# Kernel tuning notes

Measured on AMD Instinct MI355X. Metric: run time of the kernel, lower is better.

The kernel has to match this reference:

```python
import jax, jax.numpy as jnp
import numpy as np

HIDDEN = 64
LATENT = 32
HEADS = 4
EDGE_DIM = 3
NEG_SLOPE = 0.2
N_NODES = 50000
N_EDGES = 400000
IN_DIM = 128
NUM_CLASSES = 10
NUM_GRAPHS = 64


def _gatv2_layer(x, src, dst, edge_attr, Wl, Wr, We, att, b):
    # x: [N, F]; src/dst: [E] (self-loops already included); edge_attr: [E, 3]
    N = x.shape[0]
    xl = (x @ Wl).reshape(N, HEADS, HIDDEN)          # source transform (lin_l)
    xr = (x @ Wr).reshape(N, HEADS, HIDDEN)          # target transform (lin_r)
    e = (edge_attr @ We).reshape(-1, HEADS, HIDDEN)  # edge transform (lin_edge)
    s = jax.nn.leaky_relu(xl[src] + xr[dst] + e, NEG_SLOPE)   # [E,H,C]
    logits = jnp.einsum('ehc,hc->eh', s, att)                 # [E,H]
    # segment softmax over incoming edges of each destination node
    m = jax.ops.segment_max(logits, dst, num_segments=N)      # [N,H]
    ex = jnp.exp(logits - m[dst])
    denom = jax.ops.segment_sum(ex, dst, num_segments=N)      # [N,H]
    alpha = ex / denom[dst]                                   # [E,H]
    msg = xl[src] * alpha[:, :, None]                         # [E,H,C]
    out = jax.ops.segment_sum(msg, dst, num_segments=N)       # [N,H,C]
    return out.mean(axis=1) + b                               # concat=False -> head mean


def setup_inputs() -> dict:
    key = jax.random.key(0)
    ks = jax.random.split(key, 24)
    inp = {}
    inp['x'] = jax.random.normal(ks[0], (N_NODES, IN_DIM), dtype=jnp.float32)
    inp['edge_index'] = jax.random.randint(ks[1], (2, N_EDGES), 0, N_NODES)
    inp['edge_attr'] = jax.random.normal(ks[2], (N_EDGES, EDGE_DIM), dtype=jnp.float32)
    inp['batch'] = jnp.sort(jax.random.randint(ks[3], (N_NODES,), 0, NUM_GRAPHS))
    HC = HEADS * HIDDEN

    def glorot(k, shape):
        fan = shape[0] + shape[-1]
        return jax.random.normal(k, shape, dtype=jnp.float32) * jnp.sqrt(2.0 / fan)

    # layer 0 (in_dim -> hidden), layer 1 (hidden -> hidden)
    inp['Wl0'] = glorot(ks[4], (IN_DIM, HC)); inp['Wr0'] = glorot(ks[5], (IN_DIM, HC))
    inp['We0'] = glorot(ks[6], (EDGE_DIM, HC)); inp['att0'] = glorot(ks[7], (HEADS, HIDDEN))
    inp['b0'] = jnp.zeros((HIDDEN,), jnp.float32)
    inp['Wl1'] = glorot(ks[8], (HIDDEN, HC)); inp['Wr1'] = glorot(ks[9], (HIDDEN, HC))
    inp['We1'] = glorot(ks[10], (EDGE_DIM, HC)); inp['att1'] = glorot(ks[11], (HEADS, HIDDEN))
    inp['b1'] = jnp.zeros((HIDDEN,), jnp.float32)
    inp['W_mu'] = glorot(ks[12], (HIDDEN, LATENT)); inp['b_mu'] = jnp.zeros((LATENT,), jnp.float32)
    inp['W_dec'] = glorot(ks[13], (LATENT, IN_DIM)); inp['b_dec'] = jnp.zeros((IN_DIM,), jnp.float32)
    inp['W_cls'] = glorot(ks[14], (LATENT, NUM_CLASSES)); inp['b_cls'] = jnp.zeros((NUM_CLASSES,), jnp.float32)
    inp['weight'] = jax.random.normal(ks[15], (LATENT,), dtype=jnp.float32)
    return inp


def reference(x, edge_index, edge_attr, batch,
              Wl0, Wr0, We0, att0, b0,
              Wl1, Wr1, We1, att1, b1,
              W_mu, b_mu, W_dec, b_dec, W_cls, b_cls, weight):
    N = x.shape[0]
    # add self-loops once (PyG add_self_loops=True; edge_attr fill_value='mean')
    loops = jnp.arange(N, dtype=edge_index.dtype)
    src = jnp.concatenate([edge_index[0], loops])
    dst = jnp.concatenate([edge_index[1], loops])
    ea_mean = jnp.mean(edge_attr, axis=0)
    ea = jnp.concatenate([edge_attr, jnp.broadcast_to(ea_mean, (N, EDGE_DIM))], axis=0)

    h = jax.nn.relu(_gatv2_layer(x, src, dst, ea, Wl0, Wr0, We0, att0, b0))
    h = jax.nn.relu(_gatv2_layer(h, src, dst, ea, Wl1, Wr1, We1, att1, b1))
    z = h @ W_mu + b_mu                                   # [N, LATENT]

    recon = z @ W_dec + b_dec                             # node_recon: [N, in_dim]
    link = jnp.sum(z[edge_index[0]] * z[edge_index[1]] * weight, axis=1)  # [E]
    g_emb = jax.ops.segment_sum(z, batch, num_segments=NUM_GRAPHS)        # global_add_pool
    logits = g_emb @ W_cls + b_cls                        # [G, num_classes]
    return z, recon, link, logits
```

## Files before the change

kernel.cpp:

```cpp
#include <hip/hip_runtime.h>
#include <math.h>

#define HIDDEN 64
#define LATENT 32
#define HEADS 4
#define IN_DIM 128
#define NUM_CLASSES 10
#define NUM_GRAPHS 64
#define NEG_SLOPE 0.2f
#define HC 256

__global__ void k_easum(const float* __restrict__ ea, int E, float* __restrict__ ea_sum) {
    float s0 = 0.f, s1 = 0.f, s2 = 0.f;
    for (int e = blockIdx.x * blockDim.x + threadIdx.x; e < E; e += gridDim.x * blockDim.x) {
        s0 += ea[e * 3 + 0];
        s1 += ea[e * 3 + 1];
        s2 += ea[e * 3 + 2];
    }
    for (int off = 32; off; off >>= 1) {
        s0 += __shfl_xor(s0, off);
        s1 += __shfl_xor(s1, off);
        s2 += __shfl_xor(s2, off);
    }
    if ((threadIdx.x & 63) == 0) {
        atomicAdd(&ea_sum[0], s0);
        atomicAdd(&ea_sum[1], s1);
        atomicAdd(&ea_sum[2], s2);
    }
}

__global__ void k_hist(const int* __restrict__ ei, int* __restrict__ deg, int E0) {
    int e = blockIdx.x * blockDim.x + threadIdx.x;
    if (e < E0) atomicAdd(&deg[ei[E0 + e]], 1);
}

__global__ void k_scan1(const int* __restrict__ deg, int* __restrict__ off,
                        int* __restrict__ bsum, int N) {
    __shared__ int sh[256];
    int t = threadIdx.x, i = blockIdx.x * 256 + t;
    int v = (i < N) ? deg[i] : 0;
    sh[t] = v;
    __syncthreads();
    for (int d = 1; d < 256; d <<= 1) {
        int x = (t >= d) ? sh[t - d] : 0;
        __syncthreads();
        sh[t] += x;
        __syncthreads();
    }
    if (i < N) off[i] = sh[t] - v;
    if (t == 255) bsum[blockIdx.x] = sh[255];
}

__global__ void k_scan2(int* __restrict__ bsum, int nb) {
    __shared__ int sh[256];
    int t = threadIdx.x;
    int v = (t < nb) ? bsum[t] : 0;
    sh[t] = v;
    __syncthreads();
    for (int d = 1; d < 256; d <<= 1) {
        int x = (t >= d) ? sh[t - d] : 0;
        __syncthreads();
        sh[t] += x;
        __syncthreads();
    }
    if (t < nb) bsum[t] = sh[t] - v;
}

__global__ void k_scan3(int* __restrict__ off, const int* __restrict__ bsum,
                        int* __restrict__ cur, int N) {
    int i = blockIdx.x * 256 + threadIdx.x;
    if (i >= N) return;
    int o = off[i] + bsum[blockIdx.x];
    off[i] = o;
    cur[i] = o;
}

__global__ void k_scatter(const int* __restrict__ ei, const float* __restrict__ ea,
                          int* __restrict__ cur, int* __restrict__ csr_src,
                          float4* __restrict__ csr_a, int E0) {
    int e = blockIdx.x * blockDim.x + threadIdx.x;
    if (e >= E0) return;
    int dst = ei[E0 + e];
    int pos = atomicAdd(&cur[dst], 1);
    csr_src[pos] = ei[e];
    csr_a[pos] = make_float4(ea[e * 3], ea[e * 3 + 1], ea[e * 3 + 2], 0.f);
}

template <int K>
__global__ __launch_bounds__(256, 2) void k_gemm(const float* __restrict__ X,
                                                 const float* __restrict__ Wl,
                                                 const float* __restrict__ Wr,
                                                 float* __restrict__ xl, float* __restrict__ xr,
                                                 int N) {
    constexpr int KC = 64;
    constexpr int PAD = 132;
    __shared__ float sx[KC * PAD];

    const int M0 = blockIdx.x * 128;
    const int nt = blockIdx.y;
    const float* W = ((nt < 2) ? Wl : Wr) + (nt & 1) * 128;
    float* out = ((nt < 2) ? xl : xr) + (nt & 1) * 128;

    const int t = threadIdx.x;
    const int tr = t >> 4;
    const int tc = t & 15;

    float acc[8][8];
#pragma unroll
    for (int i = 0; i < 8; i++)
#pragma unroll
        for (int j = 0; j < 8; j++) acc[i][j] = 0.f;

    const int kq = t & 15;
    const int nsub = t >> 4;

    for (int kc0 = 0; kc0 < K; kc0 += KC) {
        __syncthreads();
#pragma unroll
        for (int pass = 0; pass < 8; ++pass) {
            int node = pass * 16 + nsub;
            int gn = M0 + node;
            float4 v = make_float4(0.f, 0.f, 0.f, 0.f);
            if (gn < N) v = ((const float4*)(X + (size_t)gn * K + kc0))[kq];
            int k = kq * 4;
            sx[(k + 0) * PAD + node] = v.x;
            sx[(k + 1) * PAD + node] = v.y;
            sx[(k + 2) * PAD + node] = v.z;
            sx[(k + 3) * PAD + node] = v.w;
        }
        __syncthreads();

        const float* Wc = W + (size_t)kc0 * HC;
#pragma unroll 4
        for (int k = 0; k < KC; ++k) {
            float4 a0 = *(const float4*)&sx[k * PAD + tr * 8];
            float4 a1 = *(const float4*)&sx[k * PAD + tr * 8 + 4];
            float4 b0 = *(const float4*)&Wc[(size_t)k * HC + tc * 8];
            float4 b1 = *(const float4*)&Wc[(size_t)k * HC + tc * 8 + 4];
            float a[8] = {a0.x, a0.y, a0.z, a0.w, a1.x, a1.y, a1.z, a1.w};
            float b[8] = {b0.x, b0.y, b0.z, b0.w, b1.x, b1.y, b1.z, b1.w};
#pragma unroll
            for (int i = 0; i < 8; i++)
#pragma unroll
                for (int j = 0; j < 8; j++) acc[i][j] += a[i] * b[j];
        }
    }

#pragma unroll
    for (int i = 0; i < 8; i++) {
        int gn = M0 + tr * 8 + i;
        if (gn < N) {
            float* p = out + (size_t)gn * HC + tc * 8;
            ((float4*)p)[0] = make_float4(acc[i][0], acc[i][1], acc[i][2], acc[i][3]);
            ((float4*)p)[1] = make_float4(acc[i][4], acc[i][5], acc[i][6], acc[i][7]);
        }
    }
}

__global__ void k_gat(const float* __restrict__ xl, const float* __restrict__ xr,
                      const int* __restrict__ csr_src, const float4* __restrict__ csr_a,
                      const int* __restrict__ off, const int* __restrict__ deg,
                      const float* __restrict__ easum, float invE,
                      const float* __restrict__ We, const float* __restrict__ att,
                      const float* __restrict__ bias, float* __restrict__ out, int N) {
    int wid = (blockIdx.x * blockDim.x + threadIdx.x) >> 6;
    int L = threadIdx.x & 63;
    if (wid >= N) return;
    int n = wid;

    float4 xr4 = ((const float4*)(xr + (size_t)n * HC))[L];
    float4 w0 = ((const float4*)We)[L];
    float4 w1 = ((const float4*)(We + HC))[L];
    float4 w2 = ((const float4*)(We + 2 * HC))[L];
    float4 at = ((const float4*)att)[L];
    float am0 = easum[0] * invE, am1 = easum[1] * invE, am2 = easum[2] * invE;

    float m = -INFINITY, d = 0.f;
    float acc0 = 0.f, acc1 = 0.f, acc2 = 0.f, acc3 = 0.f;
    int base = off[n], cnt = deg[n];

    for (int i = -1; i < cnt; i++) {
        int src;
        float a0, a1, a2;
        if (i < 0) {
            src = n;
            a0 = am0; a1 = am1; a2 = am2;
        } else {
            src = csr_src[base + i];
            float4 a = csr_a[base + i];
            a0 = a.x; a1 = a.y; a2 = a.z;
        }
        float4 xs = ((const float4*)(xl + (size_t)src * HC))[L];
        float s0 = xs.x + xr4.x + (a0 * w0.x + a1 * w1.x + a2 * w2.x);
        float s1 = xs.y + xr4.y + (a0 * w0.y + a1 * w1.y + a2 * w2.y);
        float s2 = xs.z + xr4.z + (a0 * w0.z + a1 * w1.z + a2 * w2.z);
        float s3 = xs.w + xr4.w + (a0 * w0.w + a1 * w1.w + a2 * w2.w);
        s0 = (s0 > 0.f) ? s0 : NEG_SLOPE * s0;
        s1 = (s1 > 0.f) ? s1 : NEG_SLOPE * s1;
        s2 = (s2 > 0.f) ? s2 : NEG_SLOPE * s2;
        s3 = (s3 > 0.f) ? s3 : NEG_SLOPE * s3;
        float p = s0 * at.x + s1 * at.y + s2 * at.z + s3 * at.w;
        p += __shfl_xor(p, 1);
        p += __shfl_xor(p, 2);
        p += __shfl_xor(p, 4);
        p += __shfl_xor(p, 8);
        float mn = fmaxf(m, p);
        float sc = __expf(m - mn);
        float ex = __expf(p - mn);
        d = d * sc + ex;
        acc0 = acc0 * sc + ex * xs.x;
        acc1 = acc1 * sc + ex * xs.y;
        acc2 = acc2 * sc + ex * xs.z;
        acc3 = acc3 * sc + ex * xs.w;
        m = mn;
    }
    float inv_d = 1.f / d;
    float v0 = acc0 * inv_d, v1 = acc1 * inv_d, v2 = acc2 * inv_d, v3 = acc3 * inv_d;
    v0 += __shfl_xor(v0, 16); v1 += __shfl_xor(v1, 16);
    v2 += __shfl_xor(v2, 16); v3 += __shfl_xor(v3, 16);
    v0 += __shfl_xor(v0, 32); v1 += __shfl_xor(v1, 32);
    v2 += __shfl_xor(v2, 32); v3 += __shfl_xor(v3, 32);
    if (L < 16) {
        float4 bx = ((const float4*)bias)[L];
        float4 o;
        o.x = fmaxf(0.25f * v0 + bx.x, 0.f);
        o.y = fmaxf(0.25f * v1 + bx.y, 0.f);
        o.z = fmaxf(0.25f * v2 + bx.z, 0.f);
        o.w = fmaxf(0.25f * v3 + bx.w, 0.f);
        ((float4*)(out + (size_t)n * HIDDEN))[L] = o;
    }
}

__global__ void k_mu(const float* __restrict__ h, const float* __restrict__ Wmu,
                     const float* __restrict__ bmu, float* __restrict__ z, int N) {
    int i = blockIdx.x * blockDim.x + threadIdx.x;
    if (i >= N * LATENT) return;
    int n = i >> 5, j = i & 31;
    const float* hr = h + (long)n * 64;
    float acc = bmu[j];
#pragma unroll
    for (int k = 0; k < 64; k++) acc += hr[k] * Wmu[k * LATENT + j];
    z[i] = acc;
}

__global__ void k_dec(const float* __restrict__ z, const float* __restrict__ W,
                      const float* __restrict__ b, float* __restrict__ out, int N) {
    int i = blockIdx.x * blockDim.x + threadIdx.x;
    if (i >= N * IN_DIM) return;
    int n = i >> 7, j = i & 127;
    const float* zr = z + (long)n * LATENT;
    float acc = b[j];
#pragma unroll
    for (int k = 0; k < LATENT; k++) acc += zr[k] * W[k * IN_DIM + j];
    out[i] = acc;
}

__global__ void k_link(const float* __restrict__ z, const int* __restrict__ ei,
                       const float* __restrict__ w, float* __restrict__ link, int E0) {
    int t = blockIdx.x * blockDim.x + threadIdx.x;
    int e = t >> 5;
    int c = t & 31;
    if (e >= E0) return;
    int s = ei[e], d = ei[E0 + e];
    float v = z[(long)s * LATENT + c] * z[(long)d * LATENT + c] * w[c];
    for (int off = 16; off; off >>= 1) v += __shfl_xor(v, off);
    if (c == 0) link[e] = v;
}

__global__ void k_pool(const float* __restrict__ z, const int* __restrict__ batch,
                       float* __restrict__ gemb, int N) {
    int i = blockIdx.x * blockDim.x + threadIdx.x;
    if (i >= N * LATENT) return;
    int n = i >> 5, j = i & 31;
    atomicAdd(&gemb[batch[n] * LATENT + j], z[i]);
}

__global__ void k_cls(const float* __restrict__ g, const float* __restrict__ W,
                      const float* __restrict__ b, float* __restrict__ out) {
    int i = blockIdx.x * blockDim.x + threadIdx.x;
    if (i >= NUM_GRAPHS * NUM_CLASSES) return;
    int gi = i / NUM_CLASSES, j = i % NUM_CLASSES;
    float acc = b[j];
#pragma unroll
    for (int k = 0; k < LATENT; k++) acc += g[gi * LATENT + k] * W[k * NUM_CLASSES + j];
    out[i] = acc;
}

extern "C" void kernel_launch(void* const* d_in, const int* in_sizes, int n_in, void* d_out,
                              int out_size, void* d_ws, size_t ws_size, hipStream_t stream) {
    const float* x = (const float*)d_in[0];
    const int* ei = (const int*)d_in[1];
    const float* ea = (const float*)d_in[2];
    const int* batch = (const int*)d_in[3];
    const float* Wl0 = (const float*)d_in[4];
    const float* Wr0 = (const float*)d_in[5];
    const float* We0 = (const float*)d_in[6];
    const float* att0 = (const float*)d_in[7];
    const float* b0 = (const float*)d_in[8];
    const float* Wl1 = (const float*)d_in[9];
    const float* Wr1 = (const float*)d_in[10];
    const float* We1 = (const float*)d_in[11];
    const float* att1 = (const float*)d_in[12];
    const float* b1 = (const float*)d_in[13];
    const float* Wmu = (const float*)d_in[14];
    const float* bmu = (const float*)d_in[15];
    const float* Wdec = (const float*)d_in[16];
    const float* bdec = (const float*)d_in[17];
    const float* Wcls = (const float*)d_in[18];
    const float* bcls = (const float*)d_in[19];
    const float* weight = (const float*)d_in[20];

    const int N = in_sizes[0] / IN_DIM;
    const int E0 = in_sizes[1] / 2;

    float* ws = (float*)d_ws;
    size_t o = 0;
    float* A = ws + o; o += (size_t)N * HC;
    float* B = ws + o; o += (size_t)N * HC;
    float4* csr_a = (float4*)(ws + o); o += (size_t)E0 * 4;
    int* csr_src = (int*)(ws + o); o += E0;
    int* deg = (int*)(ws + o); o += N;
    int* coff = (int*)(ws + o); o += N;
    int* cur = (int*)(ws + o); o += N;
    int* bsum = (int*)(ws + o); o += 256;
    float* G = ws + o; o += (size_t)N * HIDDEN;
    float* easum = ws + o; o += 16;
    float* gemb = ws + o; o += NUM_GRAPHS * LATENT;

    float* out = (float*)d_out;
    float* z_out = out;
    float* recon_out = out + (size_t)N * LATENT;
    float* link_out = recon_out + (size_t)N * IN_DIM;
    float* logits_out = link_out + (size_t)E0;

    const int TB = 256;
    const int nb = (N + 255) / 256;
    const int nodeBlocks = (N * 64 + TB - 1) / TB;
    const float invE = 1.f / (float)E0;
    const dim3 gemmGrid((N + 127) / 128, 4);

    hipMemsetAsync(deg, 0, (size_t)N * sizeof(int), stream);
    hipMemsetAsync(easum, 0, 16 * sizeof(float), stream);
    hipMemsetAsync(gemb, 0, NUM_GRAPHS * LATENT * sizeof(float), stream);
    k_easum<<<256, TB, 0, stream>>>(ea, E0, easum);
    k_hist<<<(E0 + TB - 1) / TB, TB, 0, stream>>>(ei, deg, E0);
    k_scan1<<<nb, 256, 0, stream>>>(deg, coff, bsum, N);
    k_scan2<<<1, 256, 0, stream>>>(bsum, nb);
    k_scan3<<<nb, 256, 0, stream>>>(coff, bsum, cur, N);
    k_scatter<<<(E0 + TB - 1) / TB, TB, 0, stream>>>(ei, ea, cur, csr_src, csr_a, E0);

    k_gemm<IN_DIM><<<gemmGrid, TB, 0, stream>>>(x, Wl0, Wr0, A, B, N);
    k_gat<<<nodeBlocks, TB, 0, stream>>>(A, B, csr_src, csr_a, coff, deg, easum, invE, We0,
                                         att0, b0, G, N);

    k_gemm<HIDDEN><<<gemmGrid, TB, 0, stream>>>(G, Wl1, Wr1, A, B, N);
    k_gat<<<nodeBlocks, TB, 0, stream>>>(A, B, csr_src, csr_a, coff, deg, easum, invE, We1,
                                         att1, b1, G, N);

    k_mu<<<(N * LATENT + TB - 1) / TB, TB, 0, stream>>>(G, Wmu, bmu, z_out, N);
    k_dec<<<(N * IN_DIM + TB - 1) / TB, TB, 0, stream>>>(z_out, Wdec, bdec, recon_out, N);
    k_link<<<(E0 * 32 + TB - 1) / TB, TB, 0, stream>>>(z_out, ei, weight, link_out, E0);
    k_pool<<<(N * LATENT + TB - 1) / TB, TB, 0, stream>>>(z_out, batch, gemb, N);
    k_cls<<<(NUM_GRAPHS * NUM_CLASSES + TB - 1) / TB, TB, 0, stream>>>(gemb, Wcls, bcls,
                                                                       logits_out);
}
```

Before: 752.0 us.

## Restructure GEMM shared tile to node-major and unroll GAT edge gathers by four

The GEMM now stages X in shared memory node-major with K-chunk 32 and a +1 padding. Each thread reads contiguous row segments, and the old transposed scatter stores go away. The launch bounds hint is dropped. In the GAT kernel the self-loop is peeled out of the edge loop and the remaining edges are processed four at a time, so the four gathers of xl rows are issued before their use, giving more memory-level parallelism. Risks: the GEMM inner loop now does 8 scalar LDS reads per k instead of two float4 reads, and register pressure rises in both kernels.

```diff
diff --git a/kernel.cpp b/kernel.cpp
--- a/kernel.cpp
+++ b/kernel.cpp
@@ -87,14 +87,12 @@
 }
 
 template <int K>
-__global__ __launch_bounds__(256, 2) void k_gemm(const float* __restrict__ X,
-                                                 const float* __restrict__ Wl,
-                                                 const float* __restrict__ Wr,
-                                                 float* __restrict__ xl, float* __restrict__ xr,
-                                                 int N) {
-    constexpr int KC = 64;
-    constexpr int PAD = 132;
-    __shared__ float sx[KC * PAD];
+__global__ void k_gemm(const float* __restrict__ X, const float* __restrict__ Wl,
+                       const float* __restrict__ Wr, float* __restrict__ xl,
+                       float* __restrict__ xr, int N) {
+    constexpr int KC = 32;
+    constexpr int LDK = KC + 1;
+    __shared__ float sx[128 * LDK];
 
     const int M0 = blockIdx.x * 128;
     const int nt = blockIdx.y;
@@ -111,34 +109,41 @@
 #pragma unroll
         for (int j = 0; j < 8; j++) acc[i][j] = 0.f;
 
-    const int kq = t & 15;
-    const int nsub = t >> 4;
+    const int snode = t >> 1;
+    const int shalf = (t & 1) * 16;
 
     for (int kc0 = 0; kc0 < K; kc0 += KC) {
         __syncthreads();
-#pragma unroll
-        for (int pass = 0; pass < 8; ++pass) {
-            int node = pass * 16 + nsub;
-            int gn = M0 + node;
-            float4 v = make_float4(0.f, 0.f, 0.f, 0.f);
-            if (gn < N) v = ((const float4*)(X + (size_t)gn * K + kc0))[kq];
-            int k = kq * 4;
-            sx[(k + 0) * PAD + node] = v.x;
-            sx[(k + 1) * PAD + node] = v.y;
-            sx[(k + 2) * PAD + node] = v.z;
-            sx[(k + 3) * PAD + node] = v.w;
+        {
+            float4 v[4];
+            const float* Xp = X + (size_t)(M0 + snode) * K + kc0 + shalf;
+            if (M0 + snode < N) {
+#pragma unroll
+                for (int j = 0; j < 4; j++) v[j] = ((const float4*)Xp)[j];
+            } else {
+#pragma unroll
+                for (int j = 0; j < 4; j++) v[j] = make_float4(0.f, 0.f, 0.f, 0.f);
+            }
+            float* sp = &sx[snode * LDK + shalf];
+#pragma unroll
+            for (int j = 0; j < 4; j++) {
+                sp[j * 4 + 0] = v[j].x;
+                sp[j * 4 + 1] = v[j].y;
+                sp[j * 4 + 2] = v[j].z;
+                sp[j * 4 + 3] = v[j].w;
+            }
         }
         __syncthreads();
 
-        const float* Wc = W + (size_t)kc0 * HC;
+        const float* Wk = W + (size_t)kc0 * HC + tc * 8;
 #pragma unroll 4
         for (int k = 0; k < KC; ++k) {
-            float4 a0 = *(const float4*)&sx[k * PAD + tr * 8];
-            float4 a1 = *(const float4*)&sx[k * PAD + tr * 8 + 4];
-            float4 b0 = *(const float4*)&Wc[(size_t)k * HC + tc * 8];
-            float4 b1 = *(const float4*)&Wc[(size_t)k * HC + tc * 8 + 4];
-            float a[8] = {a0.x, a0.y, a0.z, a0.w, a1.x, a1.y, a1.z, a1.w};
-            float b[8] = {b0.x, b0.y, b0.z, b0.w, b1.x, b1.y, b1.z, b1.w};
+            float b[8];
+            *(float4*)&b[0] = *(const float4*)&Wk[(size_t)k * HC];
+            *(float4*)&b[4] = *(const float4*)&Wk[(size_t)k * HC + 4];
+            float a[8];
+#pragma unroll
+            for (int i = 0; i < 8; i++) a[i] = sx[(tr * 8 + i) * LDK + k];
 #pragma unroll
             for (int i = 0; i < 8; i++)
 #pragma unroll
@@ -155,6 +160,24 @@
             ((float4*)p)[1] = make_float4(acc[i][4], acc[i][5], acc[i][6], acc[i][7]);
         }
     }
+}
+
+__device__ __forceinline__ void gat_update(float p_part, const float4& xs, float& m, float& d,
+                                           float& acc0, float& acc1, float& acc2, float& acc3) {
+    float p = p_part;
+    p += __shfl_xor(p, 1);
+    p += __shfl_xor(p, 2);
+    p += __shfl_xor(p, 4);
+    p += __shfl_xor(p, 8);
+    float mn = fmaxf(m, p);
+    float sc = __expf(m - mn);
+    float ex = __expf(p - mn);
+    d = d * sc + ex;
+    acc0 = acc0 * sc + ex * xs.x;
+    acc1 = acc1 * sc + ex * xs.y;
+    acc2 = acc2 * sc + ex * xs.z;
+    acc3 = acc3 * sc + ex * xs.w;
+    m = mn;
 }
 
 __global__ void k_gat(const float* __restrict__ xl, const float* __restrict__ xr,
@@ -173,24 +196,14 @@
     float4 w1 = ((const float4*)(We + HC))[L];
     float4 w2 = ((const float4*)(We + 2 * HC))[L];
     float4 at = ((const float4*)att)[L];
-    float am0 = easum[0] * invE, am1 = easum[1] * invE, am2 = easum[2] * invE;
 
     float m = -INFINITY, d = 0.f;
     float acc0 = 0.f, acc1 = 0.f, acc2 = 0.f, acc3 = 0.f;
     int base = off[n], cnt = deg[n];
 
-    for (int i = -1; i < cnt; i++) {
-        int src;
-        float a0, a1, a2;
-        if (i < 0) {
-            src = n;
-            a0 = am0; a1 = am1; a2 = am2;
-        } else {
-            src = csr_src[base + i];
-            float4 a = csr_a[base + i];
-            a0 = a.x; a1 = a.y; a2 = a.z;
-        }
-        float4 xs = ((const float4*)(xl + (size_t)src * HC))[L];
+    {
+        float a0 = easum[0] * invE, a1 = easum[1] * invE, a2 = easum[2] * invE;
+        float4 xs = ((const float4*)(xl + (size_t)n * HC))[L];
         float s0 = xs.x + xr4.x + (a0 * w0.x + a1 * w1.x + a2 * w2.x);
         float s1 = xs.y + xr4.y + (a0 * w0.y + a1 * w1.y + a2 * w2.y);
         float s2 = xs.z + xr4.z + (a0 * w0.z + a1 * w1.z + a2 * w2.z);
@@ -199,21 +212,52 @@
         s1 = (s1 > 0.f) ? s1 : NEG_SLOPE * s1;
         s2 = (s2 > 0.f) ? s2 : NEG_SLOPE * s2;
         s3 = (s3 > 0.f) ? s3 : NEG_SLOPE * s3;
-        float p = s0 * at.x + s1 * at.y + s2 * at.z + s3 * at.w;
-        p += __shfl_xor(p, 1);
-        p += __shfl_xor(p, 2);
-        p += __shfl_xor(p, 4);
-        p += __shfl_xor(p, 8);
-        float mn = fmaxf(m, p);
-        float sc = __expf(m - mn);
-        float ex = __expf(p - mn);
-        d = d * sc + ex;
-        acc0 = acc0 * sc + ex * xs.x;
-        acc1 = acc1 * sc + ex * xs.y;
-        acc2 = acc2 * sc + ex * xs.z;
-        acc3 = acc3 * sc + ex * xs.w;
-        m = mn;
-    }
+        gat_update(s0 * at.x + s1 * at.y + s2 * at.z + s3 * at.w, xs, m, d, acc0, acc1, acc2,
+                   acc3);
+    }
+
+    int i = 0;
+    int cnt4 = cnt & ~3;
+    for (; i < cnt4; i += 4) {
+        int s[4];
+        float4 aa[4], xs[4];
+#pragma unroll
+        for (int u = 0; u < 4; u++) s[u] = csr_src[base + i + u];
+#pragma unroll
+        for (int u = 0; u < 4; u++) aa[u] = csr_a[base + i + u];
+#pragma unroll
+        for (int u = 0; u < 4; u++) xs[u] = ((const float4*)(xl + (size_t)s[u] * HC))[L];
+#pragma unroll
+        for (int u = 0; u < 4; u++) {
+            float a0 = aa[u].x, a1 = aa[u].y, a2 = aa[u].z;
+            float s0 = xs[u].x + xr4.x + (a0 * w0.x + a1 * w1.x + a2 * w2.x);
+            float s1 = xs[u].y + xr4.y + (a0 * w0.y + a1 * w1.y + a2 * w2.y);
+            float s2 = xs[u].z + xr4.z + (a0 * w0.z + a1 * w1.z + a2 * w2.z);
+            float s3 = xs[u].w + xr4.w + (a0 * w0.w + a1 * w1.w + a2 * w2.w);
+            s0 = (s0 > 0.f) ? s0 : NEG_SLOPE * s0;
+            s1 = (s1 > 0.f) ? s1 : NEG_SLOPE * s1;
+            s2 = (s2 > 0.f) ? s2 : NEG_SLOPE * s2;
+            s3 = (s3 > 0.f) ? s3 : NEG_SLOPE * s3;
+            gat_update(s0 * at.x + s1 * at.y + s2 * at.z + s3 * at.w, xs[u], m, d, acc0, acc1,
+                       acc2, acc3);
+        }
+    }
+    for (; i < cnt; i++) {
+        int src = csr_src[base + i];
+        float4 a = csr_a[base + i];
+        float4 xs = ((const float4*)(xl + (size_t)src * HC))[L];
+        float s0 = xs.x + xr4.x + (a.x * w0.x + a.y * w1.x + a.z * w2.x);
+        float s1 = xs.y + xr4.y + (a.x * w0.y + a.y * w1.y + a.z * w2.y);
+        float s2 = xs.z + xr4.z + (a.x * w0.z + a.y * w1.z + a.z * w2.z);
+        float s3 = xs.w + xr4.w + (a.x * w0.w + a.y * w1.w + a.z * w2.w);
+        s0 = (s0 > 0.f) ? s0 : NEG_SLOPE * s0;
+        s1 = (s1 > 0.f) ? s1 : NEG_SLOPE * s1;
+        s2 = (s2 > 0.f) ? s2 : NEG_SLOPE * s2;
+        s3 = (s3 > 0.f) ? s3 : NEG_SLOPE * s3;
+        gat_update(s0 * at.x + s1 * at.y + s2 * at.z + s3 * at.w, xs, m, d, acc0, acc1, acc2,
+                   acc3);
+    }
+
     float inv_d = 1.f / d;
     float v0 = acc0 * inv_d, v1 = acc1 * inv_d, v2 = acc2 * inv_d, v3 = acc3 * inv_d;
     v0 += __shfl_xor(v0, 16); v1 += __shfl_xor(v1, 16);
```

Result: slower. 792.1 us (+5.3%).
